# Performance work log

Hardware: AMD Instinct MI355X
Metric: run time of the kernel (lower is better)

The kernel has to match this reference:

```python
import jax, jax.numpy as jnp
import numpy as np

NUM_NODES = 262144        # 1024 graphs x 256 nodes
NODES_PER_GRAPH = 256
NUM_GRAPHS = NUM_NODES // NODES_PER_GRAPH
NUM_EDGES = 2097152       # avg degree 8
NUM_FEATURES = 9
NUM_STATIONS = 8


def setup_inputs() -> dict:
    key = jax.random.key(0)
    ks = jax.random.split(key, 12)
    # edges constrained within each graph so batched-graph semantics hold
    src_local = jax.random.randint(ks[0], (NUM_EDGES,), 0, NODES_PER_GRAPH)
    dst_local = jax.random.randint(ks[1], (NUM_EDGES,), 0, NODES_PER_GRAPH)
    graph_of_edge = jax.random.randint(ks[2], (NUM_EDGES,), 0, NUM_GRAPHS)
    offset = graph_of_edge * NODES_PER_GRAPH
    edge_index = jnp.stack([src_local + offset, dst_local + offset]).astype(jnp.int64)
    station_ids = jnp.array([0, 37, 73, 110, 146, 183, 219, 255], dtype=jnp.int64)
    s = lambda k, shape, fan_in: jax.random.normal(k, shape, jnp.float32) / np.sqrt(fan_in)
    return {
        "x": jax.random.normal(ks[3], (NUM_NODES, NUM_FEATURES), jnp.float32),
        "edge_index": edge_index,
        "station_ids": station_ids,
        "W1": s(ks[4], (NUM_FEATURES, 32), NUM_FEATURES),
        "b1": jnp.zeros((32,), jnp.float32),
        "W2": s(ks[5], (32, 64), 32),
        "b2": jnp.zeros((64,), jnp.float32),
        "fc1_W": s(ks[6], (128, 64), 128),
        "fc1_b": jnp.zeros((64,), jnp.float32),
        "fc2_W": s(ks[7], (64, 1), 64),
        "fc2_b": jnp.zeros((1,), jnp.float32),
    }


def _gcn_conv(x, W, b, src, dst, n_nodes):
    """PyG GCNConv: add self-loops, symmetric normalization, linear first."""
    h = x @ W                                              # [N, C_out]
    # degree includes the self-loop (+1), counted on target nodes
    deg = jnp.zeros((n_nodes,), h.dtype).at[dst].add(1.0) + 1.0
    dinv = jax.lax.rsqrt(deg)                              # deg >= 1, safe
    norm = dinv[src] * dinv[dst]                           # [E]
    out = jnp.zeros_like(h).at[dst].add(norm[:, None] * h[src])
    out = out + (dinv * dinv)[:, None] * h                 # self-loop term
    return out + b


def reference(x, edge_index, station_ids, W1, b1, W2, b2, fc1_W, fc1_b, fc2_W, fc2_b):
    n = x.shape[0]
    src, dst = edge_index[0], edge_index[1]
    h = jax.nn.relu(_gcn_conv(x, W1, b1, src, dst, n))     # [N, 32]
    h = jax.nn.relu(_gcn_conv(h, W2, b2, src, dst, n))     # [N, 64]
    # global mean pool per graph (batch = node_idx // NODES_PER_GRAPH)
    batch = jnp.arange(n) // NODES_PER_GRAPH
    sums = jax.ops.segment_sum(h, batch, num_segments=NUM_GRAPHS)
    counts = jax.ops.segment_sum(jnp.ones((n,), h.dtype), batch, num_segments=NUM_GRAPHS)
    global_ctx = sums / counts[:, None]                    # [B, 64]
    # per-station gather-MLP, vectorized over stations
    idx = jnp.arange(NUM_GRAPHS)[:, None] * NODES_PER_GRAPH + station_ids[None, :]  # [B, S]
    station_emb = h[idx]                                   # [B, S, 64]
    ctx = jnp.broadcast_to(global_ctx[:, None, :], station_emb.shape)
    combined = jnp.concatenate([station_emb, ctx], axis=-1)  # [B, S, 128]
    q = jax.nn.relu(combined @ fc1_W + fc1_b) @ fc2_W + fc2_b  # [B, S, 1]
    return q[..., 0]                                       # [B, S]
```

## Files before the change

### kernel.cpp

```cpp
#include <hip/hip_runtime.h>
#include <hip/hip_bf16.h>


#define NNODES 262144
#define NPG 256
#define NGRAPHS 1024
#define NEDGES 2097152
#define NFEAT 9
#define ECAP2 2560
#define T_EDGES 8192
#define NTILES (NEDGES / T_EDGES)
#define TPB 1024

typedef __hip_bfloat16 bf16;
typedef short short8 __attribute__((ext_vector_type(8)));
typedef float f32x4 __attribute__((ext_vector_type(4)));

__device__ __forceinline__ float bfbits(unsigned short u) { return __uint_as_float(((unsigned)u) << 16); }
__device__ __forceinline__ unsigned short f2bbits(float v) { bf16 b = __float2bfloat16(v); return *(unsigned short*)&b; }


__global__ void __launch_bounds__(1024) k_gsort(const int* __restrict__ src,
                                                const int* __restrict__ dst,
                                                int* __restrict__ gcur,
                                                unsigned short* __restrict__ gout) {
    __shared__ unsigned short edg[T_EDGES];
    __shared__ unsigned short pay[T_EDGES];
    __shared__ int cnt[NGRAPHS];
    __shared__ int goff[NGRAPHS];
    int t = threadIdx.x;
    int base = blockIdx.x * T_EDGES;
    cnt[t] = 0;
    __syncthreads();
    const int4* s4 = (const int4*)(src + base);
    const int4* d4 = (const int4*)(dst + base);
#pragma unroll
    for (int k = 0; k < T_EDGES / 4096; ++k) {
        int idx = k * 1024 + t;
        int4 dv = d4[idx];
        int4 sv = s4[idx];
        int i0 = idx * 4;
        edg[i0]     = (unsigned short)(dv.x >> 8);
        edg[i0 + 1] = (unsigned short)(dv.y >> 8);
        edg[i0 + 2] = (unsigned short)(dv.z >> 8);
        edg[i0 + 3] = (unsigned short)(dv.w >> 8);
        pay[i0]     = (unsigned short)(((dv.x & 255) << 8) | (sv.x & 255));
        pay[i0 + 1] = (unsigned short)(((dv.y & 255) << 8) | (sv.y & 255));
        pay[i0 + 2] = (unsigned short)(((dv.z & 255) << 8) | (sv.z & 255));
        pay[i0 + 3] = (unsigned short)(((dv.w & 255) << 8) | (sv.w & 255));
        atomicAdd(&cnt[dv.x >> 8], 1);
        atomicAdd(&cnt[dv.y >> 8], 1);
        atomicAdd(&cnt[dv.z >> 8], 1);
        atomicAdd(&cnt[dv.w >> 8], 1);
    }
    __syncthreads();
    {
        int c = cnt[t];
        goff[t] = c ? atomicAdd(&gcur[t], c) : 0;
        cnt[t] = 0;
    }
    __syncthreads();
#pragma unroll
    for (int k = 0; k < T_EDGES / 1024; ++k) {
        int i = k * 1024 + t;
        int g = edg[i];
        int pos = atomicAdd(&cnt[g], 1);
        int off = goff[g] + pos;
        if (off < ECAP2) gout[(size_t)g * ECAP2 + off] = pay[i];
    }
}


__global__ void __launch_bounds__(TPB) k_fused(
    const float* __restrict__ x, const int* __restrict__ station_ids,
    const float* __restrict__ W1, const float* __restrict__ b1,
    const float* __restrict__ W2, const float* __restrict__ b2,
    const float* __restrict__ fc1W, const float* __restrict__ fc1b,
    const float* __restrict__ fc2W, const float* __restrict__ fc2b,
    const int* __restrict__ gcnt, const unsigned short* __restrict__ gedges,
    float* __restrict__ out) {

    __shared__ __align__(16) unsigned char Ms[65536];
    __shared__ __align__(16) unsigned char BufA[17024];
    __shared__ __align__(16) unsigned char BufB[17024];
    __shared__ __align__(16) unsigned char BufC[19456];
    __shared__ __align__(16) unsigned short W2Ts[64 * 40];
    __shared__ float W1s[288];
    __shared__ float dinvs[256];
    __shared__ unsigned short Rl[260];
    __shared__ unsigned char El[ECAP2];
    __shared__ unsigned int sru[512];
    __shared__ float sts[512];
    __shared__ float meanf[64];
    __shared__ float poolf[64];
    __shared__ unsigned char stmap[256];
    __shared__ float b1s[32], b2s[64], fc1bs[64], fc2ws[64];
    __shared__ int stids[8];
    __shared__ float fc2bv;

    int t = threadIdx.x;
    int g = blockIdx.x;
    int nbase = g * NPG;
    int lane = t & 63, wvid = t >> 6;
    int m = lane & 15, quad = lane >> 4;

    float* xsf = (float*)BufC;
    unsigned short* EPa = (unsigned short*)(BufC + 9216);
    unsigned short* G1T = (unsigned short*)BufA;
    unsigned short* H1T = (unsigned short*)BufB;
    unsigned short* S2 = (unsigned short*)BufC;
    unsigned short* fc1s16 = (unsigned short*)BufA;

    int ecnt = min(gcnt[g], ECAP2);
    {
        const uint4* gev = (const uint4*)(gedges + (size_t)g * ECAP2);
        uint4* epv = (uint4*)EPa;
        for (int i = t; i < ECAP2 / 8; i += TPB) epv[i] = gev[i];
    }
    const float* xg = x + (size_t)nbase * NFEAT;
    for (int i = t; i < NPG * NFEAT; i += TPB) xsf[i] = xg[i];
    for (int i = t; i < NFEAT * 32; i += TPB) W1s[i] = W1[i];
    for (int i = t; i < 2048; i += TPB)
        W2Ts[(i >> 5) * 40 + (i & 31)] = f2bbits(W2[(i & 31) * 64 + (i >> 5)]);
    if (t < 32) b1s[t] = b1[t];
    if (t < 64) { b2s[t] = b2[t]; fc1bs[t] = fc1b[t]; fc2ws[t] = fc2W[t]; poolf[t] = 0.f; }
    if (t < 8) stids[t] = station_ids[t];
    if (t == 0) fc2bv = fc2b[0];
    if (t < 256) { stmap[t] = 255; sru[t] = 0u; }
    {
        uint4* mz = (uint4*)Ms;
        uint4 z = {0u, 0u, 0u, 0u};
        for (int i = t; i < 4096; i += TPB) mz[i] = z;
    }
    __syncthreads();
    if (t < 8) stmap[stids[t] & 255] = (unsigned char)t;

    for (int i = t; i < ecnt; i += TPB) atomicAdd(&sru[EPa[i] >> 8], 1u);
    __syncthreads();

    if (wvid == 0) {
        int b0 = sru[lane * 4], b1v = sru[lane * 4 + 1], b2v = sru[lane * 4 + 2], b3 = sru[lane * 4 + 3];
        int s = b0 + b1v + b2v + b3;
        int inc = s;
        for (int off = 1; off < 64; off <<= 1) {
            int y = __shfl_up(inc, off);
            if (lane >= off) inc += y;
        }
        int run = inc - s;
        Rl[lane * 4] = (unsigned short)run; sru[256 + lane * 4] = run;
        dinvs[lane * 4] = rsqrtf((float)(b0 + 1)); run += b0;
        Rl[lane * 4 + 1] = (unsigned short)run; sru[257 + lane * 4] = run;
        dinvs[lane * 4 + 1] = rsqrtf((float)(b1v + 1)); run += b1v;
        Rl[lane * 4 + 2] = (unsigned short)run; sru[258 + lane * 4] = run;
        dinvs[lane * 4 + 2] = rsqrtf((float)(b2v + 1)); run += b2v;
        Rl[lane * 4 + 3] = (unsigned short)run; sru[259 + lane * 4] = run;
        dinvs[lane * 4 + 3] = rsqrtf((float)(b3 + 1));
        if (lane == 63) Rl[256] = (unsigned short)inc;
    }
    __syncthreads();

    for (int i = t; i < ecnt; i += TPB) {
        unsigned short v = EPa[i];
        unsigned p = atomicAdd(&sru[256 + (v >> 8)], 1u);
        if (p < ECAP2) El[p] = (unsigned char)(v & 255);
    }
    __syncthreads();

    if (t < 512) {
        int dl = t >> 2, q = t & 3;
        int d = dl;
        float did = dinvs[d];
        if ((d >> 6) == q)
            *(unsigned short*)(Ms + dl * 512 + (((d >> 3) ^ (d & 15)) * 16) + (d & 7) * 2)
                = f2bbits(did * did);
        int r0 = Rl[d], r1 = Rl[d + 1];
        for (int e = r0; e < r1; ++e) {
            int s = El[e];
            if ((s >> 6) == q) {
                unsigned short* p =
                    (unsigned short*)(Ms + dl * 512 + (((s >> 3) ^ (d & 15)) * 16) + (s & 7) * 2);
                *p = f2bbits(bfbits(*p) + did * dinvs[s]);
            }
        }
    } else {
        int idx = t - 512;
        int n = idx >> 1, half = idx & 1;
        float xv[NFEAT];
#pragma unroll
        for (int k = 0; k < NFEAT; k++) xv[k] = xsf[n * NFEAT + k];
#pragma unroll 4
        for (int ci = 0; ci < 16; ci++) {
            int c = half * 16 + ci;
            float acc = 0.f;
#pragma unroll
            for (int k = 0; k < NFEAT; k++) acc += xv[k] * W1s[k * 32 + c];
            G1T[c * 266 + n] = f2bbits(acc);
        }
    }
    __syncthreads();

    {
        int mt = wvid >> 1, nt = wvid & 1;
        f32x4 acc = {};
        for (int kt = 0; kt < 8; ++kt) {
            short8 af = *(const short8*)(Ms + (mt * 16 + m) * 512 + (((kt * 4 + quad) ^ m) * 16));
            short8 bf = *(const short8*)(BufA + (size_t)(nt * 16 + m) * 532 + kt * 64 + quad * 16);
            acc = __builtin_amdgcn_mfma_f32_16x16x32_bf16(af, bf, acc, 0, 0, 0);
        }
        int ch = nt * 16 + m;
        float bb = b1s[ch];
#pragma unroll
        for (int r = 0; r < 4; ++r) {
            int node = mt * 16 + quad * 4 + r;
            H1T[ch * 266 + node] = f2bbits(fmaxf(acc[r] + bb, 0.f));
        }
    }
    __syncthreads();

    {
        uint4* mz = (uint4*)Ms;
        uint4 z = {0u, 0u, 0u, 0u};
        for (int i = t; i < 4096; i += TPB) mz[i] = z;
    }
    __syncthreads();
    {
        int dl = t >> 3, q = t & 7;
        int d = 128 + dl;
        float did = dinvs[d];
        if (((d & 255) >> 5) == q) {
            int sd = d & 255;
            *(unsigned short*)(Ms + dl * 512 + (((sd >> 3) ^ (d & 15)) * 16) + (sd & 7) * 2)
                = f2bbits(did * did);
        }
        int r0 = Rl[d], r1 = Rl[d + 1];
        for (int e = r0; e < r1; ++e) {
            int s = El[e];
            if ((s >> 5) == q) {
                unsigned short* p =
                    (unsigned short*)(Ms + dl * 512 + (((s >> 3) ^ (d & 15)) * 16) + (s & 7) * 2);
                *p = f2bbits(bfbits(*p) + did * dinvs[s]);
            }
        }
    }
    __syncthreads();

    {
        int mt = wvid >> 1, nt = wvid & 1;
        f32x4 acc = {};
        for (int kt = 0; kt < 8; ++kt) {
            short8 af = *(const short8*)(Ms + (mt * 16 + m) * 512 + (((kt * 4 + quad) ^ m) * 16));
            short8 bf = *(const short8*)(BufA + (size_t)(nt * 16 + m) * 532 + kt * 64 + quad * 16);
            acc = __builtin_amdgcn_mfma_f32_16x16x32_bf16(af, bf, acc, 0, 0, 0);
        }
        int ch = nt * 16 + m;
        float bb = b1s[ch];
#pragma unroll
        for (int r = 0; r < 4; ++r) {
            int node = 128 + mt * 16 + quad * 4 + r;
            H1T[ch * 266 + node] = f2bbits(fmaxf(acc[r] + bb, 0.f));
        }
    }
    __syncthreads();

    for (int i = t; i < 8192; i += TPB) fc1s16[i] = f2bbits(fc1W[i]);
    {
        int mt = wvid >> 1, nt = wvid & 1;
        f32x4 acc = {};
        for (int kt = 0; kt < 8; ++kt) {
            short8 af = *(const short8*)(Ms + (mt * 16 + m) * 512 + (((kt * 4 + quad) ^ m) * 16));
            short8 bf = *(const short8*)(BufB + (size_t)(nt * 16 + m) * 532 + kt * 64 + quad * 16);
            acc = __builtin_amdgcn_mfma_f32_16x16x32_bf16(af, bf, acc, 0, 0, 0);
        }
        int ch = nt * 16 + m;
#pragma unroll
        for (int r = 0; r < 4; ++r) {
            int node = 128 + mt * 16 + quad * 4 + r;
            S2[node * 38 + ch] = f2bbits(acc[r]);
        }
    }
    __syncthreads();

    {
        uint4* mz = (uint4*)Ms;
        uint4 z = {0u, 0u, 0u, 0u};
        for (int i = t; i < 4096; i += TPB) mz[i] = z;
    }
    __syncthreads();
    {
        int dl = t >> 3, q = t & 7;
        int d = dl;
        float did = dinvs[d];
        if ((d >> 5) == q)
            *(unsigned short*)(Ms + dl * 512 + (((d >> 3) ^ (d & 15)) * 16) + (d & 7) * 2)
                = f2bbits(did * did);
        int r0 = Rl[d], r1 = Rl[d + 1];
        for (int e = r0; e < r1; ++e) {
            int s = El[e];
            if ((s >> 5) == q) {
                unsigned short* p =
                    (unsigned short*)(Ms + dl * 512 + (((s >> 3) ^ (d & 15)) * 16) + (s & 7) * 2);
                *p = f2bbits(bfbits(*p) + did * dinvs[s]);
            }
        }
    }
    __syncthreads();

    {
        int mt = wvid >> 1, nt = wvid & 1;
        f32x4 acc = {};
        for (int kt = 0; kt < 8; ++kt) {
            short8 af = *(const short8*)(Ms + (mt * 16 + m) * 512 + (((kt * 4 + quad) ^ m) * 16));
            short8 bf = *(const short8*)(BufB + (size_t)(nt * 16 + m) * 532 + kt * 64 + quad * 16);
            acc = __builtin_amdgcn_mfma_f32_16x16x32_bf16(af, bf, acc, 0, 0, 0);
        }
        int ch = nt * 16 + m;
#pragma unroll
        for (int r = 0; r < 4; ++r) {
            int node = mt * 16 + quad * 4 + r;
            S2[node * 38 + ch] = f2bbits(acc[r]);
        }
    }
    __syncthreads();

    {
        int mt = wvid;
        short8 af = *(const short8*)(BufC + (size_t)(mt * 16 + m) * 76 + quad * 16);
#pragma unroll
        for (int ni = 0; ni < 4; ++ni) {
            short8 bf = *(const short8*)((const unsigned char*)W2Ts + (size_t)(ni * 16 + m) * 80 + quad * 16);
            f32x4 c = {};
            c = __builtin_amdgcn_mfma_f32_16x16x32_bf16(af, bf, c, 0, 0, 0);
            int ch = ni * 16 + m;
            float bb = b2s[ch];
            float hv[4];
            float p = 0.f;
#pragma unroll
            for (int r = 0; r < 4; ++r) { hv[r] = fmaxf(c[r] + bb, 0.f); p += hv[r]; }
            p += __shfl_down(p, 32);
            p += __shfl_down(p, 16);
            if (quad == 0) atomicAdd(&poolf[ch], p);
#pragma unroll
            for (int r = 0; r < 4; ++r) {
                int node = mt * 16 + quad * 4 + r;
                int si = stmap[node];
                if (si != 255) sts[si * 64 + ch] = hv[r];
            }
        }
    }
    __syncthreads();

    if (t < 64) meanf[t] = poolf[t] * (1.0f / 256.0f);
    __syncthreads();

    if (wvid < 8) {
        int l = lane;
        int si = wvid;
        const float* st = sts + si * 64;
        float acc = 0.f;
#pragma unroll 8
        for (int k = 0; k < 64; k++) acc += st[k] * bfbits(fc1s16[k * 64 + l]);
#pragma unroll 8
        for (int k = 0; k < 64; k++) acc += meanf[k] * bfbits(fc1s16[(64 + k) * 64 + l]);
        float a = fmaxf(acc + fc1bs[l], 0.f) * fc2ws[l];
        for (int off = 32; off > 0; off >>= 1) a += __shfl_down(a, off);
        if (l == 0) out[g * 8 + si] = a + fc2bv;
    }
}


extern "C" void kernel_launch(void* const* d_in, const int* in_sizes, int n_in,
                              void* d_out, int out_size, void* d_ws, size_t ws_size,
                              hipStream_t stream) {
    const float* x = (const float*)d_in[0];
    const int* ei = (const int*)d_in[1];
    const int* station_ids = (const int*)d_in[2];
    const float* W1 = (const float*)d_in[3];
    const float* b1 = (const float*)d_in[4];
    const float* W2 = (const float*)d_in[5];
    const float* bias2 = (const float*)d_in[6];
    const float* fc1W = (const float*)d_in[7];
    const float* fc1b = (const float*)d_in[8];
    const float* fc2W = (const float*)d_in[9];
    const float* fc2b = (const float*)d_in[10];
    float* out = (float*)d_out;
    (void)in_sizes; (void)n_in; (void)out_size; (void)ws_size;

    char* ws = (char*)d_ws;
    int* gcur = (int*)ws;
    unsigned short* gout = (unsigned short*)(ws + 0x2000);

    const int* esrc = ei;
    const int* edst = ei + NEDGES;

    hipMemsetAsync(gcur, 0, NGRAPHS * sizeof(int), stream);
    k_gsort<<<NTILES, 1024, 0, stream>>>(esrc, edst, gcur, gout);
    k_fused<<<NGRAPHS, TPB, 0, stream>>>(x, station_ids, W1, b1, W2, bias2,
                                         fc1W, fc1b, fc2W, fc2b, gcur, gout, out);
}
```

Before: 200.1 us.

## Shrink fused GCN kernel LDS footprint via 64x128 adjacency tiles and 512 threads

The fused per-graph kernel now uses 512 threads and builds the dense normalized adjacency in 64-row by 128-column chunks (16 KB instead of 64 KB). It interleaves building each chunk with the MFMA aggregation, and folds the second-layer W2 matmul, pooling and station extraction into each 64-node quarter using a small staging buffer. The station buffer now reuses sru. This cuts LDS per block a lot so that several blocks can be resident per CU (launch bounds ask for 4), hiding latency of the serial edge scatter. The cost is more __syncthreads barriers, adjacency rebuilt per chunk with repeated edge-list scans per thread, and half as many threads per block.

Result: slower. 236.1 us (+18.0%).

```diff
diff --git a/kernel.cpp b/kernel.cpp
--- a/kernel.cpp
+++ b/kernel.cpp
@@ -10,7 +10,7 @@
 #define ECAP2 2560
 #define T_EDGES 8192
 #define NTILES (NEDGES / T_EDGES)
-#define TPB 1024
+#define TPB 512
 
 typedef __hip_bfloat16 bf16;
 typedef short short8 __attribute__((ext_vector_type(8)));
@@ -71,7 +71,7 @@
 }
 
 
-__global__ void __launch_bounds__(TPB) k_fused(
+__global__ void __launch_bounds__(TPB, 4) k_fused(
     const float* __restrict__ x, const int* __restrict__ station_ids,
     const float* __restrict__ W1, const float* __restrict__ b1,
     const float* __restrict__ W2, const float* __restrict__ b2,
@@ -80,17 +80,16 @@
     const int* __restrict__ gcnt, const unsigned short* __restrict__ gedges,
     float* __restrict__ out) {
 
-    __shared__ __align__(16) unsigned char Ms[65536];
-    __shared__ __align__(16) unsigned char BufA[17024];
-    __shared__ __align__(16) unsigned char BufB[17024];
-    __shared__ __align__(16) unsigned char BufC[19456];
-    __shared__ __align__(16) unsigned short W2Ts[64 * 40];
+    __shared__ __align__(16) unsigned char Ms[16384];
+    __shared__ __align__(16) unsigned char BufA[16896];
+    __shared__ __align__(16) unsigned char BufB[16896];
+    __shared__ __align__(16) unsigned short S2q[64 * 34];
+    __shared__ __align__(16) unsigned short W2Ts[64 * 36];
     __shared__ float W1s[288];
     __shared__ float dinvs[256];
     __shared__ unsigned short Rl[260];
     __shared__ unsigned char El[ECAP2];
     __shared__ unsigned int sru[512];
-    __shared__ float sts[512];
     __shared__ float meanf[64];
     __shared__ float poolf[64];
     __shared__ unsigned char stmap[256];
@@ -104,34 +103,29 @@
     int lane = t & 63, wvid = t >> 6;
     int m = lane & 15, quad = lane >> 4;
 
-    float* xsf = (float*)BufC;
-    unsigned short* EPa = (unsigned short*)(BufC + 9216);
+    unsigned short* EPa = (unsigned short*)BufA;
+    float* xsf = (float*)BufB;
     unsigned short* G1T = (unsigned short*)BufA;
     unsigned short* H1T = (unsigned short*)BufB;
-    unsigned short* S2 = (unsigned short*)BufC;
     unsigned short* fc1s16 = (unsigned short*)BufA;
+    float* sts = (float*)sru;
 
     int ecnt = min(gcnt[g], ECAP2);
     {
         const uint4* gev = (const uint4*)(gedges + (size_t)g * ECAP2);
-        uint4* epv = (uint4*)EPa;
+        uint4* epv = (uint4*)BufA;
         for (int i = t; i < ECAP2 / 8; i += TPB) epv[i] = gev[i];
     }
     const float* xg = x + (size_t)nbase * NFEAT;
     for (int i = t; i < NPG * NFEAT; i += TPB) xsf[i] = xg[i];
     for (int i = t; i < NFEAT * 32; i += TPB) W1s[i] = W1[i];
     for (int i = t; i < 2048; i += TPB)
-        W2Ts[(i >> 5) * 40 + (i & 31)] = f2bbits(W2[(i & 31) * 64 + (i >> 5)]);
+        W2Ts[(i >> 5) * 36 + (i & 31)] = f2bbits(W2[(i & 31) * 64 + (i >> 5)]);
     if (t < 32) b1s[t] = b1[t];
     if (t < 64) { b2s[t] = b2[t]; fc1bs[t] = fc1b[t]; fc2ws[t] = fc2W[t]; poolf[t] = 0.f; }
     if (t < 8) stids[t] = station_ids[t];
     if (t == 0) fc2bv = fc2b[0];
     if (t < 256) { stmap[t] = 255; sru[t] = 0u; }
-    {
-        uint4* mz = (uint4*)Ms;
-        uint4 z = {0u, 0u, 0u, 0u};
-        for (int i = t; i < 4096; i += TPB) mz[i] = z;
-    }
     __syncthreads();
     if (t < 8) stmap[stids[t] & 255] = (unsigned char)t;
 
@@ -166,171 +160,104 @@
     }
     __syncthreads();
 
-    if (t < 512) {
-        int dl = t >> 2, q = t & 3;
-        int d = dl;
-        float did = dinvs[d];
-        if ((d >> 6) == q)
-            *(unsigned short*)(Ms + dl * 512 + (((d >> 3) ^ (d & 15)) * 16) + (d & 7) * 2)
-                = f2bbits(did * did);
-        int r0 = Rl[d], r1 = Rl[d + 1];
-        for (int e = r0; e < r1; ++e) {
-            int s = El[e];
-            if ((s >> 6) == q) {
-                unsigned short* p =
-                    (unsigned short*)(Ms + dl * 512 + (((s >> 3) ^ (d & 15)) * 16) + (s & 7) * 2);
-                *p = f2bbits(bfbits(*p) + did * dinvs[s]);
-            }
-        }
-    } else {
-        int idx = t - 512;
-        int n = idx >> 1, half = idx & 1;
+    {
+        int n = t >> 1, hf = t & 1;
         float xv[NFEAT];
 #pragma unroll
         for (int k = 0; k < NFEAT; k++) xv[k] = xsf[n * NFEAT + k];
 #pragma unroll 4
         for (int ci = 0; ci < 16; ci++) {
-            int c = half * 16 + ci;
+            int c = hf * 16 + ci;
             float acc = 0.f;
 #pragma unroll
             for (int k = 0; k < NFEAT; k++) acc += xv[k] * W1s[k * 32 + c];
-            G1T[c * 266 + n] = f2bbits(acc);
-        }
-    }
-    __syncthreads();
-
-    {
-        int mt = wvid >> 1, nt = wvid & 1;
+            G1T[c * 264 + n] = f2bbits(acc);
+        }
+    }
+    __syncthreads();
+
+#define BUILD_M(QT, KH)                                                         \
+    {                                                                           \
+        int dl = t >> 3, q = t & 7;                                             \
+        int d = (QT) * 64 + dl;                                                 \
+        int c0 = (2 * q) ^ (dl & 15), c1 = (2 * q + 1) ^ (dl & 15);             \
+        uint4 z = {0u, 0u, 0u, 0u};                                             \
+        *(uint4*)(Ms + dl * 256 + c0 * 16) = z;                                 \
+        *(uint4*)(Ms + dl * 256 + c1 * 16) = z;                                 \
+        float did = dinvs[d];                                                   \
+        if ((d >> 7) == (KH) && ((d >> 4) & 7) == q) {                          \
+            int sp = d & 127;                                                   \
+            *(unsigned short*)(Ms + dl * 256 + (((sp >> 3) ^ (dl & 15)) * 16) + (sp & 7) * 2) \
+                = f2bbits(did * did);                                           \
+        }                                                                       \
+        int r0 = Rl[d], r1 = Rl[d + 1];                                         \
+        for (int e = r0; e < r1; ++e) {                                         \
+            int s = El[e];                                                      \
+            if ((s >> 7) == (KH) && ((s >> 4) & 7) == q) {                      \
+                int sp = s & 127;                                               \
+                unsigned short* p =                                             \
+                    (unsigned short*)(Ms + dl * 256 + (((sp >> 3) ^ (dl & 15)) * 16) + (sp & 7) * 2); \
+                *p = f2bbits(bfbits(*p) + did * dinvs[s]);                      \
+            }                                                                   \
+        }                                                                       \
+    }
+
+    int mt = wvid >> 1, nt = wvid & 1;
+
+    for (int qt = 0; qt < 4; ++qt) {
         f32x4 acc = {};
-        for (int kt = 0; kt < 8; ++kt) {
-            short8 af = *(const short8*)(Ms + (mt * 16 + m) * 512 + (((kt * 4 + quad) ^ m) * 16));
-            short8 bf = *(const short8*)(BufA + (size_t)(nt * 16 + m) * 532 + kt * 64 + quad * 16);
-            acc = __builtin_amdgcn_mfma_f32_16x16x32_bf16(af, bf, acc, 0, 0, 0);
-        }
-        int ch = nt * 16 + m;
-        float bb = b1s[ch];
-#pragma unroll
-        for (int r = 0; r < 4; ++r) {
-            int node = mt * 16 + quad * 4 + r;
-            H1T[ch * 266 + node] = f2bbits(fmaxf(acc[r] + bb, 0.f));
-        }
-    }
-    __syncthreads();
-
-    {
-        uint4* mz = (uint4*)Ms;
-        uint4 z = {0u, 0u, 0u, 0u};
-        for (int i = t; i < 4096; i += TPB) mz[i] = z;
-    }
-    __syncthreads();
-    {
-        int dl = t >> 3, q = t & 7;
-        int d = 128 + dl;
-        float did = dinvs[d];
-        if (((d & 255) >> 5) == q) {
-            int sd = d & 255;
-            *(unsigned short*)(Ms + dl * 512 + (((sd >> 3) ^ (d & 15)) * 16) + (sd & 7) * 2)
-                = f2bbits(did * did);
-        }
-        int r0 = Rl[d], r1 = Rl[d + 1];
-        for (int e = r0; e < r1; ++e) {
-            int s = El[e];
-            if ((s >> 5) == q) {
-                unsigned short* p =
-                    (unsigned short*)(Ms + dl * 512 + (((s >> 3) ^ (d & 15)) * 16) + (s & 7) * 2);
-                *p = f2bbits(bfbits(*p) + did * dinvs[s]);
+        for (int kh = 0; kh < 2; ++kh) {
+            BUILD_M(qt, kh)
+            __syncthreads();
+            for (int kt = 0; kt < 4; ++kt) {
+                short8 af = *(const short8*)(Ms + (mt * 16 + m) * 256 + (((kt * 4 + quad) ^ m) * 16));
+                short8 bf = *(const short8*)(BufA + (size_t)(nt * 16 + m) * 528 + kh * 256 + kt * 64 + quad * 16);
+                acc = __builtin_amdgcn_mfma_f32_16x16x32_bf16(af, bf, acc, 0, 0, 0);
             }
-        }
-    }
-    __syncthreads();
-
-    {
-        int mt = wvid >> 1, nt = wvid & 1;
+            if (kh == 0) __syncthreads();
+        }
+        {
+            int ch = nt * 16 + m;
+            float bb = b1s[ch];
+#pragma unroll
+            for (int r = 0; r < 4; ++r) {
+                int node = qt * 64 + mt * 16 + quad * 4 + r;
+                H1T[ch * 264 + node] = f2bbits(fmaxf(acc[r] + bb, 0.f));
+            }
+        }
+        __syncthreads();
+    }
+
+    for (int qt = 0; qt < 4; ++qt) {
         f32x4 acc = {};
-        for (int kt = 0; kt < 8; ++kt) {
-            short8 af = *(const short8*)(Ms + (mt * 16 + m) * 512 + (((kt * 4 + quad) ^ m) * 16));
-            short8 bf = *(const short8*)(BufA + (size_t)(nt * 16 + m) * 532 + kt * 64 + quad * 16);
-            acc = __builtin_amdgcn_mfma_f32_16x16x32_bf16(af, bf, acc, 0, 0, 0);
-        }
-        int ch = nt * 16 + m;
-        float bb = b1s[ch];
-#pragma unroll
-        for (int r = 0; r < 4; ++r) {
-            int node = 128 + mt * 16 + quad * 4 + r;
-            H1T[ch * 266 + node] = f2bbits(fmaxf(acc[r] + bb, 0.f));
-        }
-    }
-    __syncthreads();
-
-    for (int i = t; i < 8192; i += TPB) fc1s16[i] = f2bbits(fc1W[i]);
-    {
-        int mt = wvid >> 1, nt = wvid & 1;
-        f32x4 acc = {};
-        for (int kt = 0; kt < 8; ++kt) {
-            short8 af = *(const short8*)(Ms + (mt * 16 + m) * 512 + (((kt * 4 + quad) ^ m) * 16));
-            short8 bf = *(const short8*)(BufB + (size_t)(nt * 16 + m) * 532 + kt * 64 + quad * 16);
-            acc = __builtin_amdgcn_mfma_f32_16x16x32_bf16(af, bf, acc, 0, 0, 0);
-        }
-        int ch = nt * 16 + m;
-#pragma unroll
-        for (int r = 0; r < 4; ++r) {
-            int node = 128 + mt * 16 + quad * 4 + r;
-            S2[node * 38 + ch] = f2bbits(acc[r]);
-        }
-    }
-    __syncthreads();
-
-    {
-        uint4* mz = (uint4*)Ms;
-        uint4 z = {0u, 0u, 0u, 0u};
-        for (int i = t; i < 4096; i += TPB) mz[i] = z;
-    }
-    __syncthreads();
-    {
-        int dl = t >> 3, q = t & 7;
-        int d = dl;
-        float did = dinvs[d];
-        if ((d >> 5) == q)
-            *(unsigned short*)(Ms + dl * 512 + (((d >> 3) ^ (d & 15)) * 16) + (d & 7) * 2)
-                = f2bbits(did * did);
-        int r0 = Rl[d], r1 = Rl[d + 1];
-        for (int e = r0; e < r1; ++e) {
-            int s = El[e];
-            if ((s >> 5) == q) {
-                unsigned short* p =
-                    (unsigned short*)(Ms + dl * 512 + (((s >> 3) ^ (d & 15)) * 16) + (s & 7) * 2);
-                *p = f2bbits(bfbits(*p) + did * dinvs[s]);
+        for (int kh = 0; kh < 2; ++kh) {
+            BUILD_M(qt, kh)
+            if (qt == 0 && kh == 0)
+                for (int i = t; i < 8192; i += TPB) fc1s16[i] = f2bbits(fc1W[i]);
+            __syncthreads();
+            for (int kt = 0; kt < 4; ++kt) {
+                short8 af = *(const short8*)(Ms + (mt * 16 + m) * 256 + (((kt * 4 + quad) ^ m) * 16));
+                short8 bf = *(const short8*)(BufB + (size_t)(nt * 16 + m) * 528 + kh * 256 + kt * 64 + quad * 16);
+                acc = __builtin_amdgcn_mfma_f32_16x16x32_bf16(af, bf, acc, 0, 0, 0);
             }
-        }
-    }
-    __syncthreads();
-
-    {
-        int mt = wvid >> 1, nt = wvid & 1;
-        f32x4 acc = {};
-        for (int kt = 0; kt < 8; ++kt) {
-            short8 af = *(const short8*)(Ms + (mt * 16 + m) * 512 + (((kt * 4 + quad) ^ m) * 16));
-            short8 bf = *(const short8*)(BufB + (size_t)(nt * 16 + m) * 532 + kt * 64 + quad * 16);
-            acc = __builtin_amdgcn_mfma_f32_16x16x32_bf16(af, bf, acc, 0, 0, 0);
-        }
-        int ch = nt * 16 + m;
-#pragma unroll
-        for (int r = 0; r < 4; ++r) {
-            int node = mt * 16 + quad * 4 + r;
-            S2[node * 38 + ch] = f2bbits(acc[r]);
-        }
-    }
-    __syncthreads();
-
-    {
-        int mt = wvid;
-        short8 af = *(const short8*)(BufC + (size_t)(mt * 16 + m) * 76 + quad * 16);
-#pragma unroll
-        for (int ni = 0; ni < 4; ++ni) {
-            short8 bf = *(const short8*)((const unsigned char*)W2Ts + (size_t)(ni * 16 + m) * 80 + quad * 16);
+            if (kh == 0) __syncthreads();
+        }
+        {
+            int ch = nt * 16 + m;
+#pragma unroll
+            for (int r = 0; r < 4; ++r)
+                S2q[(mt * 16 + quad * 4 + r) * 34 + ch] = f2bbits(acc[r]);
+        }
+        __syncthreads();
+#pragma unroll
+        for (int j = 0; j < 2; ++j) {
+            int tau = wvid * 2 + j;
+            int mt2 = tau >> 2, ot = tau & 3;
+            short8 af = *(const short8*)((const unsigned char*)S2q + (size_t)(mt2 * 16 + m) * 68 + quad * 16);
+            short8 bf = *(const short8*)((const unsigned char*)W2Ts + (size_t)(ot * 16 + m) * 72 + quad * 16);
             f32x4 c = {};
             c = __builtin_amdgcn_mfma_f32_16x16x32_bf16(af, bf, c, 0, 0, 0);
-            int ch = ni * 16 + m;
+            int ch = ot * 16 + m;
             float bb = b2s[ch];
             float hv[4];
             float p = 0.f;
@@ -341,18 +268,18 @@
             if (quad == 0) atomicAdd(&poolf[ch], p);
 #pragma unroll
             for (int r = 0; r < 4; ++r) {
-                int node = mt * 16 + quad * 4 + r;
+                int node = qt * 64 + mt2 * 16 + quad * 4 + r;
                 int si = stmap[node];
                 if (si != 255) sts[si * 64 + ch] = hv[r];
             }
         }
-    }
-    __syncthreads();
+        __syncthreads();
+    }
 
     if (t < 64) meanf[t] = poolf[t] * (1.0f / 256.0f);
     __syncthreads();
 
-    if (wvid < 8) {
+    {
         int l = lane;
         int si = wvid;
         const float* st = sts + si * 64;
@@ -365,6 +292,7 @@
         for (int off = 32; off > 0; off >>= 1) a += __shfl_down(a, off);
         if (l == 0) out[g * 8 + si] = a + fc2bv;
     }
+#undef BUILD_M
 }
 
 
```
